# Optimization experiments

Hardware: AMD Instinct MI355X
Metric: run time of the kernel (lower is better)

## Reference

```python
import jax, jax.numpy as jnp
import numpy as np

N_NODES = 50000
N_GRAPHS = 128
N_FEATS = 128
HIDDEN = 128
FC_HID = 64
N_CLASSES = 10
N_EDGES = 600000


def gcn_conv(x, W, b, src, dst, n):
    # x: [N, Fin] -> [N, Fout]; symmetric-normalized scatter aggregation (PyG GCNConv)
    h = x @ W  # [N, Fout]
    ones = jnp.ones(src.shape[0], dtype=h.dtype)
    deg = jax.ops.segment_sum(ones, dst, num_segments=n)  # in-degree incl. self loops
    dinv = jnp.where(deg > 0, jax.lax.rsqrt(jnp.maximum(deg, 1.0)), 0.0)
    norm = dinv[src] * dinv[dst]  # [E]
    msg = norm[:, None] * h[src]  # gather + scale, [E, Fout]
    out = jax.ops.segment_sum(msg, dst, num_segments=n)  # scatter-add
    return out + b


def setup_inputs() -> dict:
    key = jax.random.key(0)
    ks = jax.random.split(key, 16)
    x = jax.random.normal(ks[0], (N_NODES, N_FEATS), dtype=jnp.float32)
    edge_index = jax.random.randint(ks[1], (2, N_EDGES), 0, N_NODES, dtype=jnp.int64)
    batch = jnp.sort(jax.random.randint(ks[2], (N_NODES,), 0, N_GRAPHS, dtype=jnp.int64))

    def lin(k, fin, fout):
        s = 1.0 / np.sqrt(fin)
        kw, kb = jax.random.split(k)
        W = jax.random.uniform(kw, (fin, fout), jnp.float32, -s, s)
        b = jax.random.uniform(kb, (fout,), jnp.float32, -s, s)
        return W, b

    W1, b1 = lin(ks[3], N_FEATS, HIDDEN)
    W2, b2 = lin(ks[4], HIDDEN, HIDDEN)
    W3, b3 = lin(ks[5], HIDDEN, HIDDEN)
    Wf1, bf1 = lin(ks[6], HIDDEN, FC_HID)
    Wf2, bf2 = lin(ks[7], FC_HID, N_CLASSES)
    return {"x": x, "edge_index": edge_index, "batch": batch,
            "W1": W1, "b1": b1, "W2": W2, "b2": b2, "W3": W3, "b3": b3,
            "Wf1": Wf1, "bf1": bf1, "Wf2": Wf2, "bf2": bf2}


def reference(x, edge_index, batch, W1, b1, W2, b2, W3, b3, Wf1, bf1, Wf2, bf2):
    n = x.shape[0]
    # add self loops (PyG GCNConv default)
    loop = jnp.arange(n, dtype=edge_index.dtype)
    src = jnp.concatenate([edge_index[0], loop])
    dst = jnp.concatenate([edge_index[1], loop])

    h = jax.nn.relu(gcn_conv(x, W1, b1, src, dst, n))
    h = jax.nn.relu(gcn_conv(h, W2, b2, src, dst, n))
    h = jax.nn.relu(gcn_conv(h, W3, b3, src, dst, n))

    # global mean pool per graph
    sums = jax.ops.segment_sum(h, batch, num_segments=N_GRAPHS)
    cnts = jax.ops.segment_sum(jnp.ones((n,), h.dtype), batch, num_segments=N_GRAPHS)
    hg = sums / jnp.maximum(cnts, 1.0)[:, None]  # [G, HIDDEN]

    h = jax.nn.relu(hg @ Wf1 + bf1)
    return h @ Wf2 + bf2  # [G, N_CLASSES]
```

## Files before the change

kernel.cpp:

```cpp
#include <hip/hip_runtime.h>

#define NFEAT 128
#define NGRAPHS 128
#define FCH 64
#define NCLS 10
#define ELLW 48

__global__ void ell_fill_kernel(const int* __restrict__ src, const int* __restrict__ dst, int E,
                                int* __restrict__ cursor, int* __restrict__ ell) {
    int i = (blockIdx.x * blockDim.x + threadIdx.x) * 4;
    if (i + 3 < E) {
        int4 s4 = *(const int4*)(src + i);
        int4 d4 = *(const int4*)(dst + i);
        int p;
        p = atomicAdd(&cursor[d4.x], 1); if (p < ELLW) ell[(size_t)d4.x * ELLW + p] = s4.x;
        p = atomicAdd(&cursor[d4.y], 1); if (p < ELLW) ell[(size_t)d4.y * ELLW + p] = s4.y;
        p = atomicAdd(&cursor[d4.z], 1); if (p < ELLW) ell[(size_t)d4.z * ELLW + p] = s4.z;
        p = atomicAdd(&cursor[d4.w], 1); if (p < ELLW) ell[(size_t)d4.w * ELLW + p] = s4.w;
    } else {
        for (int j = i; j < E; ++j) {
            int d = dst[j];
            int p = atomicAdd(&cursor[d], 1);
            if (p < ELLW) ell[(size_t)d * ELLW + p] = src[j];
        }
    }
}

__global__ void dinv_kernel(const int* __restrict__ deg, float* __restrict__ dinv, int N) {
    int i = blockIdx.x * blockDim.x + threadIdx.x;
    if (i < N) dinv[i] = rsqrtf((float)(deg[i] + 1));
}

__global__ __launch_bounds__(256)
void gemm128_kernel(const float* __restrict__ X, const float* __restrict__ W,
                    const float* __restrict__ dinv, float* __restrict__ H, int N) {
    __shared__ float Ws[128 * 128];
    int t = threadIdx.x;
    {
        const float4* W4 = (const float4*)W;
        float4* Ws4 = (float4*)Ws;
        #pragma unroll
        for (int i = 0; i < 16; ++i) Ws4[t + i * 256] = W4[t + i * 256];
    }
    __syncthreads();

    int tx = t & 15;
    int ty = t >> 4;
    int r0 = blockIdx.x * 128 + ty * 8;

    const float* xr[8];
    bool rowok[8];
    #pragma unroll
    for (int i = 0; i < 8; ++i) {
        rowok[i] = (r0 + i < N);
        xr[i] = X + (size_t)(rowok[i] ? (r0 + i) : 0) * NFEAT;
    }

    float acc[8][8];
    #pragma unroll
    for (int i = 0; i < 8; ++i)
        #pragma unroll
        for (int j = 0; j < 8; ++j) acc[i][j] = 0.f;

    for (int k = 0; k < 128; k += 4) {
        float xk[8][4];
        #pragma unroll
        for (int i = 0; i < 8; ++i) {
            float4 v = *(const float4*)(xr[i] + k);
            xk[i][0] = v.x; xk[i][1] = v.y; xk[i][2] = v.z; xk[i][3] = v.w;
        }
        #pragma unroll
        for (int kk = 0; kk < 4; ++kk) {
            const float* wp = &Ws[(k + kk) * 128 + (tx << 3)];
            float4 wa = *(const float4*)wp;
            float4 wb = *(const float4*)(wp + 4);
            float w[8] = {wa.x, wa.y, wa.z, wa.w, wb.x, wb.y, wb.z, wb.w};
            #pragma unroll
            for (int i = 0; i < 8; ++i) {
                float xv = xk[i][kk];
                #pragma unroll
                for (int j = 0; j < 8; ++j) acc[i][j] = fmaf(xv, w[j], acc[i][j]);
            }
        }
    }

    #pragma unroll
    for (int i = 0; i < 8; ++i) {
        if (rowok[i]) {
            float di = dinv[r0 + i];
            float* hp = H + (size_t)(r0 + i) * NFEAT + (tx << 3);
            float4 o0 = {di * acc[i][0], di * acc[i][1], di * acc[i][2], di * acc[i][3]};
            float4 o1 = {di * acc[i][4], di * acc[i][5], di * acc[i][6], di * acc[i][7]};
            *(float4*)hp = o0;
            *(float4*)(hp + 4) = o1;
        }
    }
}

__global__ __launch_bounds__(256)
void aggregate_kernel(const float* __restrict__ Hs, const int* __restrict__ deg,
                      const int* __restrict__ ell, const float* __restrict__ dinv,
                      const float* __restrict__ bias, float* __restrict__ out, int N) {
    int node = (blockIdx.x * 256 + threadIdx.x) >> 6;
    int lane = threadIdx.x & 63;
    if (node >= N) return;

    int half = lane >> 5;
    int fl = lane & 31;
    const float4* H4 = (const float4*)Hs;

    float di = dinv[node];
    float4 acc = {0.f, 0.f, 0.f, 0.f};
    if (half == 0) acc = H4[(size_t)node * 32 + fl];

    const int* row = ell + (size_t)node * ELLW;
    int d = deg[node]; if (d > ELLW) d = ELLW;
    int e = 0;

    for (; e + 7 < d; e += 8) {
        int s0 = row[e + half], s1 = row[e + 2 + half];
        int s2 = row[e + 4 + half], s3 = row[e + 6 + half];
        float4 v0 = H4[(size_t)s0 * 32 + fl];
        float4 v1 = H4[(size_t)s1 * 32 + fl];
        float4 v2 = H4[(size_t)s2 * 32 + fl];
        float4 v3 = H4[(size_t)s3 * 32 + fl];
        acc.x += v0.x + v1.x + v2.x + v3.x;
        acc.y += v0.y + v1.y + v2.y + v3.y;
        acc.z += v0.z + v1.z + v2.z + v3.z;
        acc.w += v0.w + v1.w + v2.w + v3.w;
    }
    for (; e + 1 < d; e += 2) {
        int s = row[e + half];
        float4 v = H4[(size_t)s * 32 + fl];
        acc.x += v.x; acc.y += v.y; acc.z += v.z; acc.w += v.w;
    }
    if (e < d && half == 0) {
        int s = row[e];
        float4 v = H4[(size_t)s * 32 + fl];
        acc.x += v.x; acc.y += v.y; acc.z += v.z; acc.w += v.w;
    }

    acc.x += __shfl_down(acc.x, 32, 64);
    acc.y += __shfl_down(acc.y, 32, 64);
    acc.z += __shfl_down(acc.z, 32, 64);
    acc.w += __shfl_down(acc.w, 32, 64);

    if (half == 0) {
        float4 b = ((const float4*)bias)[fl];
        float4 o;
        o.x = fmaxf(fmaf(di, acc.x, b.x), 0.f);
        o.y = fmaxf(fmaf(di, acc.y, b.y), 0.f);
        o.z = fmaxf(fmaf(di, acc.z, b.z), 0.f);
        o.w = fmaxf(fmaf(di, acc.w, b.w), 0.f);
        ((float4*)(out + (size_t)node * NFEAT))[fl] = o;
    }
}

__global__ __launch_bounds__(256)
void poolfc_kernel(const float* __restrict__ H, const int* __restrict__ batch, int N,
                   const float* __restrict__ Wf1, const float* __restrict__ bf1,
                   const float* __restrict__ Wf2, const float* __restrict__ bf2,
                   float* __restrict__ out) {
    int g = blockIdx.x;

    int lo = 0, hi = N;
    while (lo < hi) { int mid = (lo + hi) >> 1; if (batch[mid] < g) lo = mid + 1; else hi = mid; }
    int start = lo;
    hi = N;
    while (lo < hi) { int mid = (lo + hi) >> 1; if (batch[mid] < g + 1) lo = mid + 1; else hi = mid; }
    int end = lo;

    int wave = threadIdx.x >> 6;
    int lane = threadIdx.x & 63;

    float2 acc = {0.f, 0.f};
    for (int i = start + wave; i < end; i += 4) {
        float2 v = ((const float2*)(H + (size_t)i * NFEAT))[lane];
        acc.x += v.x; acc.y += v.y;
    }

    __shared__ float2 part[4][64];
    __shared__ float hg[NFEAT];
    __shared__ float h1[FCH];
    part[wave][lane] = acc;
    __syncthreads();

    if (wave == 0) {
        float2 t0 = part[0][lane], t1 = part[1][lane], t2 = part[2][lane], t3 = part[3][lane];
        float c = fmaxf((float)(end - start), 1.0f);
        hg[lane * 2]     = (t0.x + t1.x + t2.x + t3.x) / c;
        hg[lane * 2 + 1] = (t0.y + t1.y + t2.y + t3.y) / c;
        float a = bf1[lane];
        #pragma unroll 4
        for (int k = 0; k < NFEAT; ++k) a = fmaf(hg[k], Wf1[k * FCH + lane], a);
        h1[lane] = fmaxf(a, 0.f);
        if (lane < NCLS) {
            float o = bf2[lane];
            #pragma unroll
            for (int j = 0; j < FCH; ++j) o = fmaf(h1[j], Wf2[j * NCLS + lane], o);
            out[g * NCLS + lane] = o;
        }
    }
}

extern "C" void kernel_launch(void* const* d_in, const int* in_sizes, int n_in,
                              void* d_out, int out_size, void* d_ws, size_t ws_size,
                              hipStream_t stream) {
    const float* x   = (const float*)d_in[0];
    const int*   ei  = (const int*)d_in[1];
    const int*   bat = (const int*)d_in[2];
    const float* W1  = (const float*)d_in[3];
    const float* b1  = (const float*)d_in[4];
    const float* W2  = (const float*)d_in[5];
    const float* b2  = (const float*)d_in[6];
    const float* W3  = (const float*)d_in[7];
    const float* b3  = (const float*)d_in[8];
    const float* Wf1 = (const float*)d_in[9];
    const float* bf1 = (const float*)d_in[10];
    const float* Wf2 = (const float*)d_in[11];
    const float* bf2 = (const float*)d_in[12];
    float* out = (float*)d_out;

    int N = in_sizes[0] / NFEAT;
    int E = in_sizes[1] / 2;
    const int* src = ei;
    const int* dst = ei + E;

    char* ws = (char*)d_ws;
    size_t off = 0;
    auto align256 = [](size_t v) { return (v + 255) & ~(size_t)255; };

    int* cursor = (int*)(ws + off);
    off = align256(off + (size_t)N * 4);
    int* ell = (int*)(ws + off);
    off = align256(off + (size_t)N * ELLW * 4);
    float* dinv = (float*)(ws + off);
    off = align256(off + (size_t)N * 4);
    float* h0 = (float*)(ws + off);
    off = align256(off + (size_t)N * NFEAT * 4);
    float* h1 = (float*)(ws + off);
    off = align256(off + (size_t)N * NFEAT * 4);

    hipMemsetAsync(cursor, 0, (size_t)N * 4, stream);

    int tpb = 256;
    int e4blocks = ((E + 3) / 4 + tpb - 1) / tpb;
    int nblocks = (N + tpb - 1) / tpb;

    ell_fill_kernel<<<e4blocks, tpb, 0, stream>>>(src, dst, E, cursor, ell);
    dinv_kernel<<<nblocks, tpb, 0, stream>>>(cursor, dinv, N);

    int gemm_blocks = (N + 127) / 128;
    int agg_blocks = (N + 3) / 4;

    gemm128_kernel<<<gemm_blocks, 256, 0, stream>>>(x, W1, dinv, h0, N);
    aggregate_kernel<<<agg_blocks, 256, 0, stream>>>(h0, cursor, ell, dinv, b1, h1, N);
    gemm128_kernel<<<gemm_blocks, 256, 0, stream>>>(h1, W2, dinv, h0, N);
    aggregate_kernel<<<agg_blocks, 256, 0, stream>>>(h0, cursor, ell, dinv, b2, h1, N);
    gemm128_kernel<<<gemm_blocks, 256, 0, stream>>>(h1, W3, dinv, h0, N);
    aggregate_kernel<<<agg_blocks, 256, 0, stream>>>(h0, cursor, ell, dinv, b3, h1, N);

    poolfc_kernel<<<NGRAPHS, 256, 0, stream>>>(h1, bat, N, Wf1, bf1, Wf2, bf2, out);
}
```

Measured before the change: 393.2 us.

## Slice hidden features into column-sliced layout for cache-local aggregation gather

Result: slower. 553.8 us (+40.8%).

```diff
diff --git a/kernel.cpp b/kernel.cpp
--- a/kernel.cpp
+++ b/kernel.cpp
@@ -5,6 +5,9 @@
 #define FCH 64
 #define NCLS 10
 #define ELLW 48
+#define NSL 8
+#define SLF 16
+#define AGG_CH 64
 
 __global__ void ell_fill_kernel(const int* __restrict__ src, const int* __restrict__ dst, int E,
                                 int* __restrict__ cursor, int* __restrict__ ell) {
@@ -33,7 +36,7 @@
 
 __global__ __launch_bounds__(256)
 void gemm128_kernel(const float* __restrict__ X, const float* __restrict__ W,
-                    const float* __restrict__ dinv, float* __restrict__ H, int N) {
+                    const float* __restrict__ dinv, float* __restrict__ Hs, int N) {
     __shared__ float Ws[128 * 128];
     int t = threadIdx.x;
     {
@@ -84,11 +87,13 @@
         }
     }
 
+    int sl = tx >> 1;
+    int ofs = (tx & 1) * 8;
     #pragma unroll
     for (int i = 0; i < 8; ++i) {
         if (rowok[i]) {
             float di = dinv[r0 + i];
-            float* hp = H + (size_t)(r0 + i) * NFEAT + (tx << 3);
+            float* hp = Hs + ((size_t)sl * N + (r0 + i)) * SLF + ofs;
             float4 o0 = {di * acc[i][0], di * acc[i][1], di * acc[i][2], di * acc[i][3]};
             float4 o1 = {di * acc[i][4], di * acc[i][5], di * acc[i][6], di * acc[i][7]};
             *(float4*)hp = o0;
@@ -101,58 +106,49 @@
 void aggregate_kernel(const float* __restrict__ Hs, const int* __restrict__ deg,
                       const int* __restrict__ ell, const float* __restrict__ dinv,
                       const float* __restrict__ bias, float* __restrict__ out, int N) {
-    int node = (blockIdx.x * 256 + threadIdx.x) >> 6;
+    int s = blockIdx.x & (NSL - 1);
+    int chunk = blockIdx.x >> 3;
+    int wave = threadIdx.x >> 6;
     int lane = threadIdx.x & 63;
-    if (node >= N) return;
-
-    int half = lane >> 5;
-    int fl = lane & 31;
-    const float4* H4 = (const float4*)Hs;
-
-    float di = dinv[node];
-    float4 acc = {0.f, 0.f, 0.f, 0.f};
-    if (half == 0) acc = H4[(size_t)node * 32 + fl];
-
-    const int* row = ell + (size_t)node * ELLW;
-    int d = deg[node]; if (d > ELLW) d = ELLW;
-    int e = 0;
-
-    for (; e + 7 < d; e += 8) {
-        int s0 = row[e + half], s1 = row[e + 2 + half];
-        int s2 = row[e + 4 + half], s3 = row[e + 6 + half];
-        float4 v0 = H4[(size_t)s0 * 32 + fl];
-        float4 v1 = H4[(size_t)s1 * 32 + fl];
-        float4 v2 = H4[(size_t)s2 * 32 + fl];
-        float4 v3 = H4[(size_t)s3 * 32 + fl];
-        acc.x += v0.x + v1.x + v2.x + v3.x;
-        acc.y += v0.y + v1.y + v2.y + v3.y;
-        acc.z += v0.z + v1.z + v2.z + v3.z;
-        acc.w += v0.w + v1.w + v2.w + v3.w;
-    }
-    for (; e + 1 < d; e += 2) {
-        int s = row[e + half];
-        float4 v = H4[(size_t)s * 32 + fl];
-        acc.x += v.x; acc.y += v.y; acc.z += v.z; acc.w += v.w;
-    }
-    if (e < d && half == 0) {
-        int s = row[e];
-        float4 v = H4[(size_t)s * 32 + fl];
-        acc.x += v.x; acc.y += v.y; acc.z += v.z; acc.w += v.w;
-    }
-
-    acc.x += __shfl_down(acc.x, 32, 64);
-    acc.y += __shfl_down(acc.y, 32, 64);
-    acc.z += __shfl_down(acc.z, 32, 64);
-    acc.w += __shfl_down(acc.w, 32, 64);
-
-    if (half == 0) {
-        float4 b = ((const float4*)bias)[fl];
-        float4 o;
-        o.x = fmaxf(fmaf(di, acc.x, b.x), 0.f);
-        o.y = fmaxf(fmaf(di, acc.y, b.y), 0.f);
-        o.z = fmaxf(fmaf(di, acc.z, b.z), 0.f);
-        o.w = fmaxf(fmaf(di, acc.w, b.w), 0.f);
-        ((float4*)(out + (size_t)node * NFEAT))[fl] = o;
+    int eg = lane >> 2;
+    int q = lane & 3;
+
+    const float4* Hq = (const float4*)(Hs + (size_t)s * N * SLF);
+    float4 bsl = ((const float4*)bias)[s * 4 + q];
+
+    int n0 = chunk * AGG_CH;
+    int n1 = n0 + AGG_CH; if (n1 > N) n1 = N;
+
+    for (int node = n0 + wave; node < n1; node += 4) {
+        int d = deg[node]; if (d > ELLW) d = ELLW;
+        const int* row = ell + (size_t)node * ELLW;
+
+        float4 acc = {0.f, 0.f, 0.f, 0.f};
+        for (int base = 0; base < d; base += 16) {
+            int e = base + eg;
+            if (e < d) {
+                int sidx = row[e];
+                float4 v = Hq[(size_t)sidx * 4 + q];
+                acc.x += v.x; acc.y += v.y; acc.z += v.z; acc.w += v.w;
+            }
+        }
+        #pragma unroll
+        for (int m = 4; m <= 32; m <<= 1) {
+            acc.x += __shfl_xor(acc.x, m, 64);
+            acc.y += __shfl_xor(acc.y, m, 64);
+            acc.z += __shfl_xor(acc.z, m, 64);
+            acc.w += __shfl_xor(acc.w, m, 64);
+        }
+        if (eg == 0) {
+            float di = dinv[node];
+            float4 self = Hq[(size_t)node * 4 + q];
+            float4 o;
+            o.x = fmaxf(fmaf(di, acc.x + self.x, bsl.x), 0.f);
+            o.y = fmaxf(fmaf(di, acc.y + self.y, bsl.y), 0.f);
+            o.z = fmaxf(fmaf(di, acc.z + self.z, bsl.z), 0.f);
+            o.w = fmaxf(fmaf(di, acc.w + self.w, bsl.w), 0.f);
+            ((float4*)(out + (size_t)node * NFEAT + s * SLF))[q] = o;
+        }
     }
 }
 
@@ -251,7 +247,7 @@
     dinv_kernel<<<nblocks, tpb, 0, stream>>>(cursor, dinv, N);
 
     int gemm_blocks = (N + 127) / 128;
-    int agg_blocks = (N + 3) / 4;
+    int agg_blocks = ((N + AGG_CH - 1) / AGG_CH) * NSL;
 
     gemm128_kernel<<<gemm_blocks, 256, 0, stream>>>(x, W1, dinv, h0, N);
     aggregate_kernel<<<agg_blocks, 256, 0, stream>>>(h0, cursor, ell, dinv, b1, h1, N);
```
